# Optimization experiments

Hardware: AMD Instinct MI355X
Metric: run time of the kernel (lower is better)

Reference implementation:

```python
import jax, jax.numpy as jnp
import numpy as np

B, H, S, DK = 2, 16, 2048, 64

def setup_inputs() -> dict:
    key = jax.random.key(0)
    kq, kk, kv = jax.random.split(key, 3)
    shape = (B, H, S, DK)
    return {
        "multi_head_q": jax.random.normal(kq, shape, dtype=jnp.float32),
        "multi_head_k": jax.random.normal(kk, shape, dtype=jnp.float32),
        "multi_head_v": jax.random.normal(kv, shape, dtype=jnp.float32),
    }

def reference(multi_head_q, multi_head_k, multi_head_v):
    d_k = multi_head_q.shape[-1]
    scale = 1.0 / jnp.sqrt(jnp.asarray(d_k, dtype=multi_head_q.dtype))
    # scores: [B, H, S, S]
    scores = jnp.einsum("bhqd,bhkd->bhqk", multi_head_q, multi_head_k) * scale
    attn = jax.nn.softmax(scores, axis=-1)
    # z: [B, H, S, DK]
    z = jnp.einsum("bhqk,bhkd->bhqd", attn, multi_head_v)
    # transpose heads to [B, S, H, DK] then merge -> [B, S, H*DK]
    b, h, s, d = z.shape
    return jnp.swapaxes(z, 1, 2).reshape(b, s, h * d)
```

## Files before the change

### kernel.cpp

```cpp
#include <hip/hip_runtime.h>
#include <cmath>


#define S_LEN   2048
#define D_HEAD  64
#define NHEADS  16
#define TQ      128
#define TK      64
#define NITER   (S_LEN / TK)
#define LDSTR   72

typedef short bfrag8 __attribute__((ext_vector_type(8)));
typedef float f32x4  __attribute__((ext_vector_type(4)));
typedef int   i32x2  __attribute__((ext_vector_type(2)));
typedef int   i32x4  __attribute__((ext_vector_type(4)));

static __device__ __forceinline__ short f2bf(float f) {
  unsigned int u = __builtin_bit_cast(unsigned int, f);
  u = (u + 0x7fffu + ((u >> 16) & 1u)) >> 16;
  return (short)(unsigned short)u;
}

static __device__ __forceinline__ int pk2bf(float a, float b) {
#if __has_builtin(__builtin_amdgcn_cvt_pk_bf16_f32)
  typedef __bf16 bf16x2 __attribute__((ext_vector_type(2)));
  bf16x2 r = __builtin_amdgcn_cvt_pk_bf16_f32(a, b);
  return __builtin_bit_cast(int, r);
#else
  return (int)(unsigned short)f2bf(a) | ((int)(unsigned short)f2bf(b) << 16);
#endif
}

static __device__ __forceinline__ float fexp2(float x) {
#if __has_builtin(__builtin_amdgcn_exp2f)
  return __builtin_amdgcn_exp2f(x);
#else
  return exp2f(x);
#endif
}

__global__ __launch_bounds__(256, 2)
void fa_fwd(const float* __restrict__ Q, const float* __restrict__ K,
            const float* __restrict__ V, float* __restrict__ Out) {
  __shared__ short Ks [2][TK     * LDSTR];
  __shared__ short VsT[2][D_HEAD * LDSTR];
  __shared__ short Ps [TQ * LDSTR];

  const int tid  = threadIdx.x;
  const int wid  = tid >> 6;
  const int lane = tid & 63;
  const int quad = lane >> 4;
  const int r    = lane & 15;
  const int qb   = 32 * wid;

  const int bh = blockIdx.y;
  const int q0 = blockIdx.x * TQ;

  const float* Qg = Q + (size_t)bh * S_LEN * D_HEAD;
  const float* Kg = K + (size_t)bh * S_LEN * D_HEAD;
  const float* Vg = V + (size_t)bh * S_LEN * D_HEAD;

  const float qscale = 0.125f * 1.44269504088896340736f;

  bfrag8 qf[2][2];
#pragma unroll
  for (int nt = 0; nt < 2; ++nt) {
#pragma unroll
    for (int ks = 0; ks < 2; ++ks) {
      const float* qp = Qg + (size_t)(q0 + qb + 16 * nt + r) * D_HEAD + 32 * ks + 8 * quad;
      float4 a = *(const float4*)qp;
      float4 b = *(const float4*)(qp + 4);
      i32x4 w;
      w[0] = pk2bf(a.x * qscale, a.y * qscale);
      w[1] = pk2bf(a.z * qscale, a.w * qscale);
      w[2] = pk2bf(b.x * qscale, b.y * qscale);
      w[3] = pk2bf(b.z * qscale, b.w * qscale);
      qf[nt][ks] = __builtin_bit_cast(bfrag8, w);
    }
  }

  float4 kpre[4];
  float  vpre[16];

  auto load_tile = [&](int k0) {
#pragma unroll
    for (int i = 0; i < 4; ++i) {
      int e = (i * 256 + tid) * 4;
      int row = e >> 6, col = e & 63;
      kpre[i] = *(const float4*)(Kg + (size_t)(k0 + row) * D_HEAD + col);
    }
    const float* vp = Vg + (size_t)(k0 + wid * 16) * D_HEAD + lane;
#pragma unroll
    for (int j = 0; j < 16; ++j) vpre[j] = vp[(size_t)j * D_HEAD];
  };

  auto store_tile = [&](short* ksb, short* vsb) {
#pragma unroll
    for (int i = 0; i < 4; ++i) {
      int e = (i * 256 + tid) * 4;
      int row = e >> 6, col = e & 63;
      i32x2 w;
      w[0] = pk2bf(kpre[i].x, kpre[i].y);
      w[1] = pk2bf(kpre[i].z, kpre[i].w);
      *(i32x2*)&ksb[row * LDSTR + col] = w;
    }
    i32x4 w0, w1;
#pragma unroll
    for (int j = 0; j < 4; ++j) w0[j] = pk2bf(vpre[2 * j],     vpre[2 * j + 1]);
#pragma unroll
    for (int j = 0; j < 4; ++j) w1[j] = pk2bf(vpre[8 + 2 * j], vpre[9 + 2 * j]);
    *(i32x4*)&vsb[lane * LDSTR + wid * 16]     = w0;
    *(i32x4*)&vsb[lane * LDSTR + wid * 16 + 8] = w1;
  };

  f32x4 acc[4][2];
#pragma unroll
  for (int mt = 0; mt < 4; ++mt)
#pragma unroll
    for (int nt = 0; nt < 2; ++nt)
      acc[mt][nt] = (f32x4){0.f, 0.f, 0.f, 0.f};

  float lrun[2] = {0.f, 0.f};

  auto compute = [&](const short* ksb, const short* vsb) {
    f32x4 st[4][2];
#pragma unroll
    for (int mt = 0; mt < 4; ++mt)
#pragma unroll
      for (int nt = 0; nt < 2; ++nt)
        st[mt][nt] = (f32x4){0.f, 0.f, 0.f, 0.f};

#pragma unroll
    for (int ks = 0; ks < 2; ++ks) {
      bfrag8 af[4];
#pragma unroll
      for (int mt = 0; mt < 4; ++mt)
        af[mt] = *(const bfrag8*)&ksb[(r + 16 * mt) * LDSTR + quad * 8 + 32 * ks];
#pragma unroll
      for (int mt = 0; mt < 4; ++mt)
#pragma unroll
        for (int nt = 0; nt < 2; ++nt)
          st[mt][nt] = __builtin_amdgcn_mfma_f32_16x16x32_bf16(af[mt], qf[nt][ks], st[mt][nt], 0, 0, 0);
    }

#pragma unroll
    for (int nt = 0; nt < 2; ++nt) {
      float ssum = 0.f;
#pragma unroll
      for (int mt = 0; mt < 4; ++mt) {
        float p0 = fexp2(st[mt][nt][0]);
        float p1 = fexp2(st[mt][nt][1]);
        float p2 = fexp2(st[mt][nt][2]);
        float p3 = fexp2(st[mt][nt][3]);
        ssum += (p0 + p1) + (p2 + p3);
        i32x2 w;
        w[0] = pk2bf(p0, p1);
        w[1] = pk2bf(p2, p3);
        *(i32x2*)&Ps[(qb + 16 * nt + r) * LDSTR + 16 * mt + 4 * quad] = w;
      }
      lrun[nt] += ssum;
    }

#pragma unroll
    for (int ks = 0; ks < 2; ++ks) {
      bfrag8 av[4], bp[2];
#pragma unroll
      for (int mt = 0; mt < 4; ++mt)
        av[mt] = *(const bfrag8*)&vsb[(r + 16 * mt) * LDSTR + quad * 8 + 32 * ks];
#pragma unroll
      for (int nt = 0; nt < 2; ++nt)
        bp[nt] = *(const bfrag8*)&Ps[(qb + 16 * nt + r) * LDSTR + quad * 8 + 32 * ks];
#pragma unroll
      for (int mt = 0; mt < 4; ++mt)
#pragma unroll
        for (int nt = 0; nt < 2; ++nt)
          acc[mt][nt] = __builtin_amdgcn_mfma_f32_16x16x32_bf16(av[mt], bp[nt], acc[mt][nt], 0, 0, 0);
    }
  };

  load_tile(0);
  store_tile(Ks[0], VsT[0]);
  load_tile(TK);

  for (int it = 0; it < NITER; it += 2) {
    __syncthreads();
    compute(Ks[0], VsT[0]);
    store_tile(Ks[1], VsT[1]);
    if (it + 2 < NITER) load_tile((it + 2) * TK);

    __syncthreads();
    compute(Ks[1], VsT[1]);
    if (it + 2 < NITER) {
      store_tile(Ks[0], VsT[0]);
      if (it + 3 < NITER) load_tile((it + 3) * TK);
    }
  }

  const int bb = bh >> 4, hh = bh & 15;
#pragma unroll
  for (int nt = 0; nt < 2; ++nt) {
    float l = lrun[nt];
    l += __shfl_xor(l, 16);
    l += __shfl_xor(l, 32);
    float inv = 1.0f / l;
    int qg = q0 + qb + 16 * nt + r;
    float* op = Out + ((size_t)bb * S_LEN + qg) * (NHEADS * D_HEAD) + hh * D_HEAD;
#pragma unroll
    for (int mt = 0; mt < 4; ++mt) {
      float4 o;
      o.x = acc[mt][nt][0] * inv; o.y = acc[mt][nt][1] * inv;
      o.z = acc[mt][nt][2] * inv; o.w = acc[mt][nt][3] * inv;
      *(float4*)(op + 16 * mt + 4 * quad) = o;
    }
  }
}

extern "C" void kernel_launch(void* const* d_in, const int* in_sizes, int n_in,
                              void* d_out, int out_size, void* d_ws, size_t ws_size,
                              hipStream_t stream) {
  const float* Q = (const float*)d_in[0];
  const float* K = (const float*)d_in[1];
  const float* V = (const float*)d_in[2];
  float* O = (float*)d_out;
  dim3 grid(S_LEN / TQ, 2 * NHEADS);
  fa_fwd<<<grid, 256, 0, stream>>>(Q, K, V, O);
}
```

Measured before the change: 146.7 us.

## Split KV sequence across two blocks and add a combine kernel

Adds a split-K variant that launches twice as many blocks, each covering half of the key/value sequence and writing unnormalized partial outputs and row sums to the workspace. A second kernel adds the two partials and normalizes them. The split kernel also switches to single-buffered LDS with an occupancy hint of 4 blocks per CU. The intent is to fill the GPU better than the original grid of 512 blocks, at the cost of extra global traffic for the partials and a second launch. The original kernel is kept as a fallback when the workspace is too small.

```diff
diff --git a/kernel.cpp b/kernel.cpp
--- a/kernel.cpp
+++ b/kernel.cpp
@@ -5,8 +5,11 @@
 #define S_LEN   2048
 #define D_HEAD  64
 #define NHEADS  16
+#define NBH     32
 #define TQ      128
 #define TK      64
+#define HALFLEN (S_LEN / 2)
+#define HITER   (HALFLEN / TK)
 #define NITER   (S_LEN / TK)
 #define LDSTR   72
 
@@ -39,12 +42,13 @@
 #endif
 }
 
-__global__ __launch_bounds__(256, 2)
-void fa_fwd(const float* __restrict__ Q, const float* __restrict__ K,
-            const float* __restrict__ V, float* __restrict__ Out) {
-  __shared__ short Ks [2][TK     * LDSTR];
-  __shared__ short VsT[2][D_HEAD * LDSTR];
-  __shared__ short Ps [TQ * LDSTR];
+__global__ __launch_bounds__(256, 4)
+void fa_fwd_sk(const float* __restrict__ Q, const float* __restrict__ K,
+               const float* __restrict__ V, float* __restrict__ Zp,
+               float* __restrict__ Lp) {
+  __shared__ short Ks [TK     * LDSTR];
+  __shared__ short VsT[D_HEAD * LDSTR];
+  __shared__ short Ps [TQ     * LDSTR];
 
   const int tid  = threadIdx.x;
   const int wid  = tid >> 6;
@@ -53,12 +57,13 @@
   const int r    = lane & 15;
   const int qb   = 32 * wid;
 
-  const int bh = blockIdx.y;
-  const int q0 = blockIdx.x * TQ;
+  const int bh   = blockIdx.y;
+  const int q0   = blockIdx.x * TQ;
+  const int half = blockIdx.z;
 
   const float* Qg = Q + (size_t)bh * S_LEN * D_HEAD;
-  const float* Kg = K + (size_t)bh * S_LEN * D_HEAD;
-  const float* Vg = V + (size_t)bh * S_LEN * D_HEAD;
+  const float* Kg = K + ((size_t)bh * S_LEN + half * HALFLEN) * D_HEAD;
+  const float* Vg = V + ((size_t)bh * S_LEN + half * HALFLEN) * D_HEAD;
 
   const float qscale = 0.125f * 1.44269504088896340736f;
 
@@ -79,22 +84,22 @@
     }
   }
 
+  const float* kp = Kg + ((tid * 4) >> 6) * D_HEAD + ((tid * 4) & 63);
+  const float* vp = Vg + (size_t)(wid * 16) * D_HEAD + lane;
+
   float4 kpre[4];
   float  vpre[16];
 
-  auto load_tile = [&](int k0) {
-#pragma unroll
-    for (int i = 0; i < 4; ++i) {
-      int e = (i * 256 + tid) * 4;
-      int row = e >> 6, col = e & 63;
-      kpre[i] = *(const float4*)(Kg + (size_t)(k0 + row) * D_HEAD + col);
-    }
-    const float* vp = Vg + (size_t)(k0 + wid * 16) * D_HEAD + lane;
-#pragma unroll
-    for (int j = 0; j < 16; ++j) vpre[j] = vp[(size_t)j * D_HEAD];
+  auto load_tile = [&]() {
+#pragma unroll
+    for (int i = 0; i < 4; ++i) kpre[i] = *(const float4*)(kp + i * (16 * D_HEAD));
+#pragma unroll
+    for (int j = 0; j < 16; ++j) vpre[j] = vp[j * D_HEAD];
+    kp += TK * D_HEAD;
+    vp += TK * D_HEAD;
   };
 
-  auto store_tile = [&](short* ksb, short* vsb) {
+  auto store_tile = [&]() {
 #pragma unroll
     for (int i = 0; i < 4; ++i) {
       int e = (i * 256 + tid) * 4;
@@ -102,15 +107,15 @@
       i32x2 w;
       w[0] = pk2bf(kpre[i].x, kpre[i].y);
       w[1] = pk2bf(kpre[i].z, kpre[i].w);
-      *(i32x2*)&ksb[row * LDSTR + col] = w;
+      *(i32x2*)&Ks[row * LDSTR + col] = w;
     }
     i32x4 w0, w1;
 #pragma unroll
     for (int j = 0; j < 4; ++j) w0[j] = pk2bf(vpre[2 * j],     vpre[2 * j + 1]);
 #pragma unroll
     for (int j = 0; j < 4; ++j) w1[j] = pk2bf(vpre[8 + 2 * j], vpre[9 + 2 * j]);
-    *(i32x4*)&vsb[lane * LDSTR + wid * 16]     = w0;
-    *(i32x4*)&vsb[lane * LDSTR + wid * 16 + 8] = w1;
+    *(i32x4*)&VsT[lane * LDSTR + wid * 16]     = w0;
+    *(i32x4*)&VsT[lane * LDSTR + wid * 16 + 8] = w1;
   };
 
   f32x4 acc[4][2];
@@ -122,7 +127,14 @@
 
   float lrun[2] = {0.f, 0.f};
 
-  auto compute = [&](const short* ksb, const short* vsb) {
+  load_tile();
+
+  for (int it = 0; it < HITER; ++it) {
+    __syncthreads();
+    store_tile();
+    if (it + 1 < HITER) load_tile();
+    __syncthreads();
+
     f32x4 st[4][2];
 #pragma unroll
     for (int mt = 0; mt < 4; ++mt)
@@ -135,7 +147,7 @@
       bfrag8 af[4];
 #pragma unroll
       for (int mt = 0; mt < 4; ++mt)
-        af[mt] = *(const bfrag8*)&ksb[(r + 16 * mt) * LDSTR + quad * 8 + 32 * ks];
+        af[mt] = *(const bfrag8*)&Ks[(r + 16 * mt) * LDSTR + quad * 8 + 32 * ks];
 #pragma unroll
       for (int mt = 0; mt < 4; ++mt)
 #pragma unroll
@@ -166,6 +178,191 @@
       bfrag8 av[4], bp[2];
 #pragma unroll
       for (int mt = 0; mt < 4; ++mt)
+        av[mt] = *(const bfrag8*)&VsT[(r + 16 * mt) * LDSTR + quad * 8 + 32 * ks];
+#pragma unroll
+      for (int nt = 0; nt < 2; ++nt)
+        bp[nt] = *(const bfrag8*)&Ps[(qb + 16 * nt + r) * LDSTR + quad * 8 + 32 * ks];
+#pragma unroll
+      for (int mt = 0; mt < 4; ++mt)
+#pragma unroll
+        for (int nt = 0; nt < 2; ++nt)
+          acc[mt][nt] = __builtin_amdgcn_mfma_f32_16x16x32_bf16(av[mt], bp[nt], acc[mt][nt], 0, 0, 0);
+    }
+  }
+
+  float* zbase = Zp + (size_t)(half * NBH + bh) * S_LEN * D_HEAD;
+  float* lbase = Lp + (size_t)(half * NBH + bh) * S_LEN;
+#pragma unroll
+  for (int nt = 0; nt < 2; ++nt) {
+    float l = lrun[nt];
+    l += __shfl_xor(l, 16);
+    l += __shfl_xor(l, 32);
+    int qg = q0 + qb + 16 * nt + r;
+    if (quad == 0) lbase[qg] = l;
+    float* op = zbase + (size_t)qg * D_HEAD;
+#pragma unroll
+    for (int mt = 0; mt < 4; ++mt) {
+      float4 o;
+      o.x = acc[mt][nt][0]; o.y = acc[mt][nt][1];
+      o.z = acc[mt][nt][2]; o.w = acc[mt][nt][3];
+      *(float4*)(op + 16 * mt + 4 * quad) = o;
+    }
+  }
+}
+
+__global__ __launch_bounds__(256)
+void fa_combine(const float* __restrict__ Zp, const float* __restrict__ Lp,
+                float* __restrict__ Out) {
+  const int t  = blockIdx.x * 256 + threadIdx.x;
+  const int d4 = t & 15;
+  const int h  = (t >> 4) & 15;
+  const int q  = (t >> 8) & 2047;
+  const int b  = t >> 19;
+  const size_t bh = (size_t)b * NHEADS + h;
+
+  const size_t zhalf = (size_t)NBH * S_LEN * D_HEAD;
+  const size_t zi = (bh * S_LEN + q) * D_HEAD + d4 * 4;
+  float4 z0 = *(const float4*)(Zp + zi);
+  float4 z1 = *(const float4*)(Zp + zhalf + zi);
+
+  const size_t li = bh * S_LEN + q;
+  float inv = 1.0f / (Lp[li] + Lp[(size_t)NBH * S_LEN + li]);
+
+  float4 o;
+  o.x = (z0.x + z1.x) * inv;
+  o.y = (z0.y + z1.y) * inv;
+  o.z = (z0.z + z1.z) * inv;
+  o.w = (z0.w + z1.w) * inv;
+  *(float4*)(Out + ((size_t)b * S_LEN + q) * (NHEADS * D_HEAD) + h * D_HEAD + d4 * 4) = o;
+}
+
+__global__ __launch_bounds__(256, 2)
+void fa_fwd(const float* __restrict__ Q, const float* __restrict__ K,
+            const float* __restrict__ V, float* __restrict__ Out) {
+  __shared__ short Ks [2][TK     * LDSTR];
+  __shared__ short VsT[2][D_HEAD * LDSTR];
+  __shared__ short Ps [TQ * LDSTR];
+
+  const int tid  = threadIdx.x;
+  const int wid  = tid >> 6;
+  const int lane = tid & 63;
+  const int quad = lane >> 4;
+  const int r    = lane & 15;
+  const int qb   = 32 * wid;
+
+  const int bh = blockIdx.y;
+  const int q0 = blockIdx.x * TQ;
+
+  const float* Qg = Q + (size_t)bh * S_LEN * D_HEAD;
+  const float* Kg = K + (size_t)bh * S_LEN * D_HEAD;
+  const float* Vg = V + (size_t)bh * S_LEN * D_HEAD;
+
+  const float qscale = 0.125f * 1.44269504088896340736f;
+
+  bfrag8 qf[2][2];
+#pragma unroll
+  for (int nt = 0; nt < 2; ++nt) {
+#pragma unroll
+    for (int ks = 0; ks < 2; ++ks) {
+      const float* qp = Qg + (size_t)(q0 + qb + 16 * nt + r) * D_HEAD + 32 * ks + 8 * quad;
+      float4 a = *(const float4*)qp;
+      float4 b = *(const float4*)(qp + 4);
+      i32x4 w;
+      w[0] = pk2bf(a.x * qscale, a.y * qscale);
+      w[1] = pk2bf(a.z * qscale, a.w * qscale);
+      w[2] = pk2bf(b.x * qscale, b.y * qscale);
+      w[3] = pk2bf(b.z * qscale, b.w * qscale);
+      qf[nt][ks] = __builtin_bit_cast(bfrag8, w);
+    }
+  }
+
+  float4 kpre[4];
+  float  vpre[16];
+
+  auto load_tile = [&](int k0) {
+#pragma unroll
+    for (int i = 0; i < 4; ++i) {
+      int e = (i * 256 + tid) * 4;
+      int row = e >> 6, col = e & 63;
+      kpre[i] = *(const float4*)(Kg + (size_t)(k0 + row) * D_HEAD + col);
+    }
+    const float* vpp = Vg + (size_t)(k0 + wid * 16) * D_HEAD + lane;
+#pragma unroll
+    for (int j = 0; j < 16; ++j) vpre[j] = vpp[(size_t)j * D_HEAD];
+  };
+
+  auto store_tile = [&](short* ksb, short* vsb) {
+#pragma unroll
+    for (int i = 0; i < 4; ++i) {
+      int e = (i * 256 + tid) * 4;
+      int row = e >> 6, col = e & 63;
+      i32x2 w;
+      w[0] = pk2bf(kpre[i].x, kpre[i].y);
+      w[1] = pk2bf(kpre[i].z, kpre[i].w);
+      *(i32x2*)&ksb[row * LDSTR + col] = w;
+    }
+    i32x4 w0, w1;
+#pragma unroll
+    for (int j = 0; j < 4; ++j) w0[j] = pk2bf(vpre[2 * j],     vpre[2 * j + 1]);
+#pragma unroll
+    for (int j = 0; j < 4; ++j) w1[j] = pk2bf(vpre[8 + 2 * j], vpre[9 + 2 * j]);
+    *(i32x4*)&vsb[lane * LDSTR + wid * 16]     = w0;
+    *(i32x4*)&vsb[lane * LDSTR + wid * 16 + 8] = w1;
+  };
+
+  f32x4 acc[4][2];
+#pragma unroll
+  for (int mt = 0; mt < 4; ++mt)
+#pragma unroll
+    for (int nt = 0; nt < 2; ++nt)
+      acc[mt][nt] = (f32x4){0.f, 0.f, 0.f, 0.f};
+
+  float lrun[2] = {0.f, 0.f};
+
+  auto compute = [&](const short* ksb, const short* vsb) {
+    f32x4 st[4][2];
+#pragma unroll
+    for (int mt = 0; mt < 4; ++mt)
+#pragma unroll
+      for (int nt = 0; nt < 2; ++nt)
+        st[mt][nt] = (f32x4){0.f, 0.f, 0.f, 0.f};
+
+#pragma unroll
+    for (int ks = 0; ks < 2; ++ks) {
+      bfrag8 af[4];
+#pragma unroll
+      for (int mt = 0; mt < 4; ++mt)
+        af[mt] = *(const bfrag8*)&ksb[(r + 16 * mt) * LDSTR + quad * 8 + 32 * ks];
+#pragma unroll
+      for (int mt = 0; mt < 4; ++mt)
+#pragma unroll
+        for (int nt = 0; nt < 2; ++nt)
+          st[mt][nt] = __builtin_amdgcn_mfma_f32_16x16x32_bf16(af[mt], qf[nt][ks], st[mt][nt], 0, 0, 0);
+    }
+
+#pragma unroll
+    for (int nt = 0; nt < 2; ++nt) {
+      float ssum = 0.f;
+#pragma unroll
+      for (int mt = 0; mt < 4; ++mt) {
+        float p0 = fexp2(st[mt][nt][0]);
+        float p1 = fexp2(st[mt][nt][1]);
+        float p2 = fexp2(st[mt][nt][2]);
+        float p3 = fexp2(st[mt][nt][3]);
+        ssum += (p0 + p1) + (p2 + p3);
+        i32x2 w;
+        w[0] = pk2bf(p0, p1);
+        w[1] = pk2bf(p2, p3);
+        *(i32x2*)&Ps[(qb + 16 * nt + r) * LDSTR + 16 * mt + 4 * quad] = w;
+      }
+      lrun[nt] += ssum;
+    }
+
+#pragma unroll
+    for (int ks = 0; ks < 2; ++ks) {
+      bfrag8 av[4], bp[2];
+#pragma unroll
+      for (int mt = 0; mt < 4; ++mt)
         av[mt] = *(const bfrag8*)&vsb[(r + 16 * mt) * LDSTR + quad * 8 + 32 * ks];
 #pragma unroll
       for (int nt = 0; nt < 2; ++nt)
@@ -222,6 +419,20 @@
   const float* K = (const float*)d_in[1];
   const float* V = (const float*)d_in[2];
   float* O = (float*)d_out;
-  dim3 grid(S_LEN / TQ, 2 * NHEADS);
-  fa_fwd<<<grid, 256, 0, stream>>>(Q, K, V, O);
-}
+
+  const size_t zelems = (size_t)2 * NBH * S_LEN * D_HEAD;
+  const size_t lelems = (size_t)2 * NBH * S_LEN;
+  const size_t need   = (zelems + lelems) * sizeof(float);
+
+  if (ws_size >= need) {
+    float* Zp = (float*)d_ws;
+    float* Lp = Zp + zelems;
+    dim3 g1(S_LEN / TQ, NBH, 2);
+    fa_fwd_sk<<<g1, 256, 0, stream>>>(Q, K, V, Zp, Lp);
+    const int n4 = (2 * S_LEN * NHEADS * D_HEAD) / 4;
+    fa_combine<<<n4 / 256, 256, 0, stream>>>(Zp, Lp, O);
+  } else {
+    dim3 grid(S_LEN / TQ, NBH);
+    fa_fwd<<<grid, 256, 0, stream>>>(Q, K, V, O);
+  }
+}
```

After: 196.8 us. 34.2% more time.
